# Kernel optimization log

Measured on AMD Instinct MI355X. Metric: run time of the kernel, lower is better.

The kernel has to match this reference:

```python
import jax, jax.numpy as jnp
import numpy as np

NUM_SEQS = 128
TOTAL_TOKENS = 65536
HIDDEN = 768
FF = 3072
EPS = 1e-12  # torch F.normalize default eps


def _make_prompt_lens(rng: np.random.Generator) -> np.ndarray:
    # Ragged lengths in [64, 960], adjusted so they sum exactly to TOTAL_TOKENS.
    lens = rng.integers(64, 960, size=NUM_SEQS).astype(np.int64)
    lens = np.maximum(1, (lens * (TOTAL_TOKENS / lens.sum())).astype(np.int64))
    lens[-1] += TOTAL_TOKENS - lens.sum()
    assert lens.sum() == TOTAL_TOKENS and (lens > 0).all()
    return lens


def setup_inputs() -> dict:
    key = jax.random.key(0)
    k1, k2, k3 = jax.random.split(key, 3)
    hidden_states = jax.random.normal(k1, (TOTAL_TOKENS, HIDDEN), dtype=jnp.float32)
    prompt_lens = jnp.asarray(_make_prompt_lens(np.random.default_rng(0)))
    W1 = jax.random.normal(k2, (FF, HIDDEN), dtype=jnp.float32) * (HIDDEN ** -0.5)
    W2 = jax.random.normal(k3, (HIDDEN, FF), dtype=jnp.float32) * (FF ** -0.5)
    return {"hidden_states": hidden_states, "prompt_lens": prompt_lens, "W1": W1, "W2": W2}


def reference(hidden_states, prompt_lens, W1, W2):
    # hidden_states: [T, H]; prompt_lens: [S] summing to T.
    T = hidden_states.shape[0]
    S = prompt_lens.shape[0]
    # segment id of each token: index of first cumsum strictly greater than position
    seg_ids = jnp.searchsorted(jnp.cumsum(prompt_lens), jnp.arange(T), side="right")
    sums = jax.ops.segment_sum(hidden_states, seg_ids, num_segments=S)  # [S, H]
    pooled = sums / prompt_lens[:, None].astype(hidden_states.dtype)     # mean pool
    h = jnp.einsum("sh,fh->sf", pooled, W1)   # dense1: 768 -> 3072 (no bias)
    h = jnp.einsum("sf,hf->sh", h, W2)        # dense2: 3072 -> 768 (no bias)
    norm = jnp.linalg.norm(h, ord=2, axis=-1, keepdims=True)
    return h / jnp.maximum(norm, EPS)         # L2 normalize, [S, H]
```

## Files before the change

### kernel.cpp

```cpp
#include <hip/hip_runtime.h>

#define TOK   65536
#define HID   768
#define NSEQ  128
#define FFD   3072
#define CHUNK 128
#define POOL_THREADS 192
#define KC 16

__device__ __forceinline__ void add4(float4& a, const float4 b) {
  a.x += b.x; a.y += b.y; a.z += b.z; a.w += b.w;
}

__global__ __launch_bounds__(POOL_THREADS) void pool_kernel(
    const float* __restrict__ x, const int* __restrict__ lens,
    float* __restrict__ pooled) {
  const int t0 = blockIdx.x * CHUNK;
  const int t1 = t0 + CHUNK;
  const int col = threadIdx.x;

  int seg = 0, cum = 0;
  int L = lens[0];
  while (cum + L <= t0) { cum += L; ++seg; L = lens[seg]; }

  const float4* xv = (const float4*)x + col;
  int t = t0;
  while (t < t1) {
    const int seg_end = cum + L;
    const int run_end = seg_end < t1 ? seg_end : t1;
    const int n = run_end - t;
    const float4* p = xv + (size_t)t * (HID / 4);
    float4 a0 = make_float4(0.f,0.f,0.f,0.f), a1 = a0, a2 = a0, a3 = a0;
    int i = 0;
    for (; i + 4 <= n; i += 4) {
      add4(a0, p[(size_t)(i+0) * (HID/4)]);
      add4(a1, p[(size_t)(i+1) * (HID/4)]);
      add4(a2, p[(size_t)(i+2) * (HID/4)]);
      add4(a3, p[(size_t)(i+3) * (HID/4)]);
    }
    for (; i < n; ++i) add4(a0, p[(size_t)i * (HID/4)]);
    add4(a0, a1); add4(a2, a3); add4(a0, a2);

    const float inv = 1.0f / (float)L;
    float* dst = pooled + (size_t)seg * HID + col * 4;
    atomicAdd(dst + 0, a0.x * inv);
    atomicAdd(dst + 1, a0.y * inv);
    atomicAdd(dst + 2, a0.z * inv);
    atomicAdd(dst + 3, a0.w * inv);

    t = run_end;
    if (run_end == seg_end) {
      cum = seg_end; ++seg;
      if (seg < NSEQ) L = lens[seg];
    }
  }
}

__global__ __launch_bounds__(256) void gemm_nt(
    const float* __restrict__ A, const float* __restrict__ B,
    float* __restrict__ C, int N, int Kt, int Kchunk) {
  __shared__ float As[KC][132];
  __shared__ float Bs[KC][34];

  const int tid = threadIdx.x;
  const int f0 = blockIdx.x * 32;
  const int k0 = blockIdx.y * Kchunk;
  int kend = k0 + Kchunk; if (kend > Kt) kend = Kt;
  const int fx = (tid & 15) * 2;
  const int sy = (tid >> 4) * 8;

  float acc[8][2];
  #pragma unroll
  for (int i = 0; i < 8; ++i) { acc[i][0] = 0.f; acc[i][1] = 0.f; }

  for (int kc = k0; kc < kend; kc += KC) {
    #pragma unroll
    for (int r = 0; r < 8; ++r) {
      int l = tid + 256 * r;
      int s = l >> 4, kk = l & 15;
      As[kk][s] = A[(size_t)s * Kt + kc + kk];
    }
    #pragma unroll
    for (int r = 0; r < 2; ++r) {
      int l = tid + 256 * r;
      int f = l >> 4, kk = l & 15;
      Bs[kk][f] = B[(size_t)(f0 + f) * Kt + kc + kk];
    }
    __syncthreads();
    #pragma unroll
    for (int kk = 0; kk < KC; ++kk) {
      const float4 aA = *(const float4*)&As[kk][sy];
      const float4 aB = *(const float4*)&As[kk][sy + 4];
      const float2 bb = *(const float2*)&Bs[kk][fx];
      acc[0][0] += aA.x*bb.x; acc[0][1] += aA.x*bb.y;
      acc[1][0] += aA.y*bb.x; acc[1][1] += aA.y*bb.y;
      acc[2][0] += aA.z*bb.x; acc[2][1] += aA.z*bb.y;
      acc[3][0] += aA.w*bb.x; acc[3][1] += aA.w*bb.y;
      acc[4][0] += aB.x*bb.x; acc[4][1] += aB.x*bb.y;
      acc[5][0] += aB.y*bb.x; acc[5][1] += aB.y*bb.y;
      acc[6][0] += aB.z*bb.x; acc[6][1] += aB.z*bb.y;
      acc[7][0] += aB.w*bb.x; acc[7][1] += aB.w*bb.y;
    }
    __syncthreads();
  }
  #pragma unroll
  for (int i = 0; i < 8; ++i) {
    float* cp = C + (size_t)(sy + i) * N + f0 + fx;
    atomicAdd(cp + 0, acc[i][0]);
    atomicAdd(cp + 1, acc[i][1]);
  }
}

__global__ __launch_bounds__(256) void l2norm_kernel(float* __restrict__ out) {
  const int s = blockIdx.x;
  float* row = out + (size_t)s * HID;
  const int tid = threadIdx.x;
  float v0 = row[tid], v1 = row[tid + 256], v2 = row[tid + 512];
  float ss = v0*v0 + v1*v1 + v2*v2;
  #pragma unroll
  for (int off = 32; off > 0; off >>= 1) ss += __shfl_down(ss, off, 64);
  __shared__ float wsum[4];
  if ((tid & 63) == 0) wsum[tid >> 6] = ss;
  __syncthreads();
  const float tot = wsum[0] + wsum[1] + wsum[2] + wsum[3];
  const float scale = 1.0f / fmaxf(sqrtf(tot), 1e-12f);
  row[tid] = v0 * scale;
  row[tid + 256] = v1 * scale;
  row[tid + 512] = v2 * scale;
}

extern "C" void kernel_launch(void* const* d_in, const int* in_sizes, int n_in,
                              void* d_out, int out_size, void* d_ws, size_t ws_size,
                              hipStream_t stream) {
  const float* x    = (const float*)d_in[0];
  const int*   lens = (const int*)d_in[1];
  const float* W1   = (const float*)d_in[2];
  const float* W2   = (const float*)d_in[3];
  float* out = (float*)d_out;

  float* pooled = (float*)d_ws;
  float* h1     = pooled + NSEQ * HID;

  hipMemsetAsync(d_ws, 0, (size_t)(NSEQ * HID + NSEQ * FFD) * sizeof(float), stream);
  hipMemsetAsync(d_out, 0, (size_t)NSEQ * HID * sizeof(float), stream);

  pool_kernel<<<TOK / CHUNK, POOL_THREADS, 0, stream>>>(x, lens, pooled);
  gemm_nt<<<dim3(FFD / 32, 2), 256, 0, stream>>>(pooled, W1, h1, FFD, HID, 384);
  gemm_nt<<<dim3(HID / 32, 8), 256, 0, stream>>>(h1, W2, out, HID, FFD, 384);
  l2norm_kernel<<<NSEQ, 256, 0, stream>>>(out);
}
```

Measured before the change: 358.8 us.

## Replace atomic split-K with partial buffers, widen GEMM tiles, precompute segment starts

A new prep kernel computes an inclusive scan of the sequence lengths and a per-chunk starting segment, so each pool block skips the serial linear search, and the pool chunk size is halved to launch more blocks. The GEMMs now write split-K partials to separate buffers with plain float4 stores instead of atomics. The next stage sums those partials while loading its A tile, and the norm kernel sums the second GEMM's partials itself. GEMM tiles widen to 64 output columns with float4 vectorized loads. This removes most memsets and atomic traffic, at the cost of extra partial-buffer reads and one more small launch.

```diff
diff --git a/kernel.cpp b/kernel.cpp
--- a/kernel.cpp
+++ b/kernel.cpp
@@ -4,24 +4,50 @@
 #define HID   768
 #define NSEQ  128
 #define FFD   3072
-#define CHUNK 128
-#define POOL_THREADS 192
-#define KC 16
+#define CHUNK 64
+#define NCHUNK (TOK / CHUNK)
+#define KS1 5
+#define KS2 20
+#define KCH 160
 
 __device__ __forceinline__ void add4(float4& a, const float4 b) {
   a.x += b.x; a.y += b.y; a.z += b.z; a.w += b.w;
 }
 
-__global__ __launch_bounds__(POOL_THREADS) void pool_kernel(
+__global__ __launch_bounds__(256) void prep_kernel(
+    const int* __restrict__ lens, int* __restrict__ incl,
+    int* __restrict__ start_seg) {
+  __shared__ int sc[NSEQ];
+  const int t = threadIdx.x;
+  if (t < NSEQ) sc[t] = lens[t];
+  __syncthreads();
+  for (int off = 1; off < NSEQ; off <<= 1) {
+    int v = 0;
+    if (t < NSEQ && t >= off) v = sc[t - off];
+    __syncthreads();
+    if (t < NSEQ) sc[t] += v;
+    __syncthreads();
+  }
+  if (t < NSEQ) incl[t] = sc[t];
+  for (int c = t; c < NCHUNK; c += 256) {
+    const int t0 = c * CHUNK;
+    int lo = 0, hi = NSEQ - 1;
+    while (lo < hi) { int mid = (lo + hi) >> 1; if (sc[mid] <= t0) lo = mid + 1; else hi = mid; }
+    start_seg[c] = lo;
+  }
+}
+
+__global__ __launch_bounds__(192) void pool_kernel(
     const float* __restrict__ x, const int* __restrict__ lens,
+    const int* __restrict__ incl, const int* __restrict__ start_seg,
     float* __restrict__ pooled) {
   const int t0 = blockIdx.x * CHUNK;
   const int t1 = t0 + CHUNK;
   const int col = threadIdx.x;
 
-  int seg = 0, cum = 0;
-  int L = lens[0];
-  while (cum + L <= t0) { cum += L; ++seg; L = lens[seg]; }
+  int seg = start_seg[blockIdx.x];
+  int L = lens[seg];
+  int cum = incl[seg] - L;
 
   const float4* xv = (const float4*)x + col;
   int t = t0;
@@ -58,65 +84,82 @@
 
 __global__ __launch_bounds__(256) void gemm_nt(
     const float* __restrict__ A, const float* __restrict__ B,
-    float* __restrict__ C, int N, int Kt, int Kchunk) {
-  __shared__ float As[KC][132];
-  __shared__ float Bs[KC][34];
+    float* __restrict__ Cp, int N, int Kt, int nsum, int pstride) {
+  __shared__ float As[16][132];
+  __shared__ float Bs[16][68];
 
   const int tid = threadIdx.x;
-  const int f0 = blockIdx.x * 32;
-  const int k0 = blockIdx.y * Kchunk;
-  int kend = k0 + Kchunk; if (kend > Kt) kend = Kt;
-  const int fx = (tid & 15) * 2;
+  const int f0 = blockIdx.x * 64;
+  const int k0 = blockIdx.y * KCH;
+  const int kend = (k0 + KCH) < Kt ? (k0 + KCH) : Kt;
+  float* C = Cp + (size_t)blockIdx.y * NSEQ * N;
+  const int fx = (tid & 15) * 4;
   const int sy = (tid >> 4) * 8;
 
-  float acc[8][2];
+  float acc[8][4];
   #pragma unroll
-  for (int i = 0; i < 8; ++i) { acc[i][0] = 0.f; acc[i][1] = 0.f; }
+  for (int i = 0; i < 8; ++i)
+    #pragma unroll
+    for (int j = 0; j < 4; ++j) acc[i][j] = 0.f;
 
-  for (int kc = k0; kc < kend; kc += KC) {
-    #pragma unroll
-    for (int r = 0; r < 8; ++r) {
-      int l = tid + 256 * r;
-      int s = l >> 4, kk = l & 15;
-      As[kk][s] = A[(size_t)s * Kt + kc + kk];
-    }
+  for (int kc = k0; kc < kend; kc += 16) {
     #pragma unroll
     for (int r = 0; r < 2; ++r) {
-      int l = tid + 256 * r;
-      int f = l >> 4, kk = l & 15;
-      Bs[kk][f] = B[(size_t)(f0 + f) * Kt + kc + kk];
+      const int l = tid + 256 * r;
+      const int s = l >> 2, k4 = (l & 3) * 4;
+      const float* ap = A + (size_t)s * Kt + kc + k4;
+      float4 v = *(const float4*)ap;
+      for (int p = 1; p < nsum; ++p) {
+        const float4 w = *(const float4*)(ap + (size_t)p * pstride);
+        add4(v, w);
+      }
+      As[k4 + 0][s] = v.x; As[k4 + 1][s] = v.y;
+      As[k4 + 2][s] = v.z; As[k4 + 3][s] = v.w;
+    }
+    {
+      const int f = tid >> 2, k4 = (tid & 3) * 4;
+      const float4 v = *(const float4*)(B + (size_t)(f0 + f) * Kt + kc + k4);
+      Bs[k4 + 0][f] = v.x; Bs[k4 + 1][f] = v.y;
+      Bs[k4 + 2][f] = v.z; Bs[k4 + 3][f] = v.w;
     }
     __syncthreads();
     #pragma unroll
-    for (int kk = 0; kk < KC; ++kk) {
+    for (int kk = 0; kk < 16; ++kk) {
       const float4 aA = *(const float4*)&As[kk][sy];
       const float4 aB = *(const float4*)&As[kk][sy + 4];
-      const float2 bb = *(const float2*)&Bs[kk][fx];
-      acc[0][0] += aA.x*bb.x; acc[0][1] += aA.x*bb.y;
-      acc[1][0] += aA.y*bb.x; acc[1][1] += aA.y*bb.y;
-      acc[2][0] += aA.z*bb.x; acc[2][1] += aA.z*bb.y;
-      acc[3][0] += aA.w*bb.x; acc[3][1] += aA.w*bb.y;
-      acc[4][0] += aB.x*bb.x; acc[4][1] += aB.x*bb.y;
-      acc[5][0] += aB.y*bb.x; acc[5][1] += aB.y*bb.y;
-      acc[6][0] += aB.z*bb.x; acc[6][1] += aB.z*bb.y;
-      acc[7][0] += aB.w*bb.x; acc[7][1] += aB.w*bb.y;
+      const float4 bb = *(const float4*)&Bs[kk][fx];
+      acc[0][0] += aA.x*bb.x; acc[0][1] += aA.x*bb.y; acc[0][2] += aA.x*bb.z; acc[0][3] += aA.x*bb.w;
+      acc[1][0] += aA.y*bb.x; acc[1][1] += aA.y*bb.y; acc[1][2] += aA.y*bb.z; acc[1][3] += aA.y*bb.w;
+      acc[2][0] += aA.z*bb.x; acc[2][1] += aA.z*bb.y; acc[2][2] += aA.z*bb.z; acc[2][3] += aA.z*bb.w;
+      acc[3][0] += aA.w*bb.x; acc[3][1] += aA.w*bb.y; acc[3][2] += aA.w*bb.z; acc[3][3] += aA.w*bb.w;
+      acc[4][0] += aB.x*bb.x; acc[4][1] += aB.x*bb.y; acc[4][2] += aB.x*bb.z; acc[4][3] += aB.x*bb.w;
+      acc[5][0] += aB.y*bb.x; acc[5][1] += aB.y*bb.y; acc[5][2] += aB.y*bb.z; acc[5][3] += aB.y*bb.w;
+      acc[6][0] += aB.z*bb.x; acc[6][1] += aB.z*bb.y; acc[6][2] += aB.z*bb.z; acc[6][3] += aB.z*bb.w;
+      acc[7][0] += aB.w*bb.x; acc[7][1] += aB.w*bb.y; acc[7][2] += aB.w*bb.z; acc[7][3] += aB.w*bb.w;
     }
     __syncthreads();
   }
   #pragma unroll
   for (int i = 0; i < 8; ++i) {
-    float* cp = C + (size_t)(sy + i) * N + f0 + fx;
-    atomicAdd(cp + 0, acc[i][0]);
-    atomicAdd(cp + 1, acc[i][1]);
+    float4 o = make_float4(acc[i][0], acc[i][1], acc[i][2], acc[i][3]);
+    *(float4*)(C + (size_t)(sy + i) * N + f0 + fx) = o;
   }
 }
 
-__global__ __launch_bounds__(256) void l2norm_kernel(float* __restrict__ out) {
+__global__ __launch_bounds__(256) void norm_kernel(
+    const float* __restrict__ outp, float* __restrict__ out) {
   const int s = blockIdx.x;
-  float* row = out + (size_t)s * HID;
   const int tid = threadIdx.x;
-  float v0 = row[tid], v1 = row[tid + 256], v2 = row[tid + 512];
-  float ss = v0*v0 + v1*v1 + v2*v2;
+  float v[3];
+  #pragma unroll
+  for (int j = 0; j < 3; ++j) {
+    const int c = tid + 256 * j;
+    float a = 0.f;
+    for (int p = 0; p < KS2; ++p)
+      a += outp[((size_t)p * NSEQ + s) * HID + c];
+    v[j] = a;
+  }
+  float ss = v[0]*v[0] + v[1]*v[1] + v[2]*v[2];
   #pragma unroll
   for (int off = 32; off > 0; off >>= 1) ss += __shfl_down(ss, off, 64);
   __shared__ float wsum[4];
@@ -124,9 +167,8 @@
   __syncthreads();
   const float tot = wsum[0] + wsum[1] + wsum[2] + wsum[3];
   const float scale = 1.0f / fmaxf(sqrtf(tot), 1e-12f);
-  row[tid] = v0 * scale;
-  row[tid + 256] = v1 * scale;
-  row[tid + 512] = v2 * scale;
+  #pragma unroll
+  for (int j = 0; j < 3; ++j) out[(size_t)s * HID + tid + 256 * j] = v[j] * scale;
 }
 
 extern "C" void kernel_launch(void* const* d_in, const int* in_sizes, int n_in,
@@ -139,13 +181,16 @@
   float* out = (float*)d_out;
 
   float* pooled = (float*)d_ws;
-  float* h1     = pooled + NSEQ * HID;
+  float* h1p    = pooled + NSEQ * HID;
+  float* outp   = h1p + (size_t)KS1 * NSEQ * FFD;
+  int*   incl   = (int*)(outp + (size_t)KS2 * NSEQ * HID);
+  int*   start_seg = incl + NSEQ;
 
-  hipMemsetAsync(d_ws, 0, (size_t)(NSEQ * HID + NSEQ * FFD) * sizeof(float), stream);
-  hipMemsetAsync(d_out, 0, (size_t)NSEQ * HID * sizeof(float), stream);
+  hipMemsetAsync(pooled, 0, (size_t)NSEQ * HID * sizeof(float), stream);
 
-  pool_kernel<<<TOK / CHUNK, POOL_THREADS, 0, stream>>>(x, lens, pooled);
-  gemm_nt<<<dim3(FFD / 32, 2), 256, 0, stream>>>(pooled, W1, h1, FFD, HID, 384);
-  gemm_nt<<<dim3(HID / 32, 8), 256, 0, stream>>>(h1, W2, out, HID, FFD, 384);
-  l2norm_kernel<<<NSEQ, 256, 0, stream>>>(out);
+  prep_kernel<<<1, 256, 0, stream>>>(lens, incl, start_seg);
+  pool_kernel<<<NCHUNK, 192, 0, stream>>>(x, lens, incl, start_seg, pooled);
+  gemm_nt<<<dim3(FFD / 64, KS1), 256, 0, stream>>>(pooled, W1, h1p, FFD, HID, 1, 0);
+  gemm_nt<<<dim3(HID / 64, KS2), 256, 0, stream>>>(h1p, W2, outp, HID, FFD, KS1, NSEQ * FFD);
+  norm_kernel<<<NSEQ, 256, 0, stream>>>(outp, out);
 }
```

After: 355.1 us. No clear change (-1.0%).
